# Optimization experiments

Measured on AMD Instinct MI355X. Metric: run time of the kernel, lower is better.

Reference implementation:

```python
import jax, jax.numpy as jnp
import numpy as np

B, S, D, H = 4, 2048, 1024, 16
DK = D // H
THETA = 10000.0


def _rope(x, pos):
    # x: [..., S, DK]; interleaved-pair rotation as in the torch module
    dk = x.shape[-1]
    inv_freq = 1.0 / (THETA ** (jnp.arange(0, dk, 2, dtype=jnp.float32) / dk))  # [dk/2]
    freqs = pos.astype(jnp.float32)[:, None] * inv_freq  # [S, dk/2]
    cos, sin = jnp.cos(freqs), jnp.sin(freqs)
    xr = x.reshape(*x.shape[:-1], dk // 2, 2)
    x0, x1 = xr[..., 0], xr[..., 1]
    rot = jnp.stack([x0 * cos - x1 * sin, x0 * sin + x1 * cos], axis=-1)
    return rot.reshape(x.shape)


def setup_inputs() -> dict:
    key = jax.random.key(0)
    ks = jax.random.split(key, 5)
    scale = 0.02
    return {
        "x": jax.random.normal(ks[0], (B, S, D), dtype=jnp.float32),
        "Wq": jax.random.normal(ks[1], (D, D), dtype=jnp.float32) * scale,
        "Wk": jax.random.normal(ks[2], (D, D), dtype=jnp.float32) * scale,
        "Wv": jax.random.normal(ks[3], (D, D), dtype=jnp.float32) * scale,
        "Wo": jax.random.normal(ks[4], (D, D), dtype=jnp.float32) * scale,
    }


def reference(x, Wq, Wk, Wv, Wo):
    b, s, d = x.shape
    pos = jnp.arange(s)
    # projections (Linear with no bias, y = x @ W^T)
    q = jnp.einsum('bsd,ed->bse', x, Wq).reshape(b, s, H, DK).transpose(0, 2, 1, 3)
    k = jnp.einsum('bsd,ed->bse', x, Wk).reshape(b, s, H, DK).transpose(0, 2, 1, 3)
    v = jnp.einsum('bsd,ed->bse', x, Wv).reshape(b, s, H, DK).transpose(0, 2, 1, 3)
    q = _rope(q, pos)
    k = _rope(k, pos)
    scores = jnp.einsum('bhqd,bhkd->bhqk', q, k) / jnp.sqrt(jnp.float32(DK))
    causal = jnp.tril(jnp.ones((s, s), dtype=bool))
    scores = jnp.where(causal, scores, -jnp.inf)
    attn = jax.nn.softmax(scores, axis=-1)
    out = jnp.einsum('bhqk,bhkd->bhqd', attn, v)
    out = out.transpose(0, 2, 1, 3).reshape(b, s, d)
    return jnp.einsum('bsd,ed->bse', out, Wo)
```

## Files before the change

### kernel.cpp

```cpp
#include <hip/hip_runtime.h>

#define B_  4
#define S_  2048
#define D_  1024
#define H_  16
#define DK_ 64
#define BH_ (B_*H_)
#define L2E 1.44269504088896f

typedef __attribute__((ext_vector_type(8))) short bf16x8;
typedef __attribute__((ext_vector_type(4))) float f32x4;
typedef __attribute__((ext_vector_type(16))) float f32x16;
typedef __attribute__((ext_vector_type(4))) unsigned u32x4;
typedef unsigned short u16;

__device__ __forceinline__ u16 f2bf(float f){
  unsigned u = __builtin_bit_cast(unsigned, f);
  u += 0x7fffu + ((u >> 16) & 1u);
  return (u16)(u >> 16);
}
__device__ __forceinline__ float bf2f(u16 h){
  unsigned u = ((unsigned)h) << 16;
  return __builtin_bit_cast(float, u);
}

#define GLD16(g,l) __builtin_amdgcn_global_load_lds( \
    (const __attribute__((address_space(1))) void*)(g), \
    (__attribute__((address_space(3))) void*)(l), 16, 0, 0)

#define MFMA16(a,b,c) __builtin_amdgcn_mfma_f32_16x16x32_bf16((a),(b),(c),0,0,0)
#define MFMA32(a,b,c) __builtin_amdgcn_mfma_f32_32x32x16_bf16((a),(b),(c),0,0,0)

__global__ void cast_kernel(const float4* __restrict__ in, ushort4* __restrict__ out, int n4){
  int i = blockIdx.x*blockDim.x + threadIdx.x;
  int stride = gridDim.x*blockDim.x;
  for (; i < n4; i += stride){
    float4 v = in[i];
    ushort4 o;
    o.x = f2bf(v.x); o.y = f2bf(v.y); o.z = f2bf(v.z); o.w = f2bf(v.w);
    out[i] = o;
  }
}

__global__ void trig_kernel(float* __restrict__ ct, float* __restrict__ st){
  int t = blockIdx.x*blockDim.x + threadIdx.x;
  int i = t & 31, s = t >> 5;
  float expo = -(float)(2*i) * (1.0f/(float)DK_);
  float inv = powf(10000.0f, expo);
  float ang = (float)s * inv;
  ct[t] = cosf(ang);
  st[t] = sinf(ang);
}

__global__ void rope_kernel(u16* __restrict__ X, const float* __restrict__ ct,
                            const float* __restrict__ st, float scale){
  int t = blockIdx.x*blockDim.x + threadIdx.x;
  int c8 = t & 7;
  int s  = (t >> 3) & (S_-1);
  bf16x8 v = *(bf16x8*)(X + (size_t)t*8);
  float4 c4 = *(const float4*)(ct + s*32 + c8*4);
  float4 s4 = *(const float4*)(st + s*32 + c8*4);
  float cc[4] = {c4.x, c4.y, c4.z, c4.w};
  float ss[4] = {s4.x, s4.y, s4.z, s4.w};
  #pragma unroll
  for (int j=0;j<4;++j){
    float x0 = bf2f((u16)v[2*j]);
    float x1 = bf2f((u16)v[2*j+1]);
    float r0 = x0*cc[j] - x1*ss[j];
    float r1 = x0*ss[j] + x1*cc[j];
    v[2*j]   = (short)f2bf(r0*scale);
    v[2*j+1] = (short)f2bf(r1*scale);
  }
  *(bf16x8*)(X + (size_t)t*8) = v;
}

template<int MODE>
__global__ __launch_bounds__(256, 2)
void gemm_bt(const u16* __restrict__ A,
             const u16* __restrict__ B0, const u16* __restrict__ B1, const u16* __restrict__ B2,
             u16* __restrict__ O0, u16* __restrict__ O1, u16* __restrict__ O2,
             float* __restrict__ Cf, int K){
  __shared__ __align__(16) u16 lA[128*64];
  __shared__ __align__(16) u16 lB[128*64];
  const u16* Bm = B0;
  u16* Om = O0;
  if (MODE == 0){
    if (blockIdx.z == 1){ Bm = B1; Om = O1; }
    else if (blockIdx.z == 2){ Bm = B2; Om = O2; }
  }
  const int m0 = blockIdx.y*128, n0 = blockIdx.x*128;
  const int tid = threadIdx.x, wave = tid>>6, lane = tid&63;
  const int wm = wave>>1, wn = wave&1;
  const int srow = lane>>3, scol = (lane&7)*8;

  f32x4 acc[4][4];
  #pragma unroll
  for (int m=0;m<4;++m)
    #pragma unroll
    for (int n=0;n<4;++n) acc[m][n] = (f32x4){0.f,0.f,0.f,0.f};

  #pragma unroll 1
  for (int k0 = 0; k0 < K; k0 += 64){
    #pragma unroll
    for (int j=0;j<4;++j){
      int rb = (wave*4 + j)*8;
      GLD16(A  + (size_t)(m0 + rb + srow)*K + k0 + scol, lA + rb*64);
      GLD16(Bm + (size_t)(n0 + rb + srow)*K + k0 + scol, lB + rb*64);
    }
    __syncthreads();
    #pragma unroll
    for (int kk=0;kk<2;++kk){
      bf16x8 af[4], bfr[4];
      #pragma unroll
      for (int m=0;m<4;++m) af[m]  = *(const bf16x8*)&lA[(wm*64 + m*16 + (lane&15))*64 + kk*32 + (lane>>4)*8];
      #pragma unroll
      for (int n=0;n<4;++n) bfr[n] = *(const bf16x8*)&lB[(wn*64 + n*16 + (lane&15))*64 + kk*32 + (lane>>4)*8];
      #pragma unroll
      for (int m=0;m<4;++m)
        #pragma unroll
        for (int n=0;n<4;++n)
          acc[m][n] = MFMA16(af[m], bfr[n], acc[m][n]);
    }
    __syncthreads();
  }

  #pragma unroll
  for (int m=0;m<4;++m){
    const int rb = m0 + wm*64 + m*16 + ((lane>>4)<<2);
    #pragma unroll
    for (int n=0;n<4;++n){
      const int e = n0 + wn*64 + n*16 + (lane&15);
      if (MODE == 0){
        const int h = e>>6, dk = e&63;
        if (blockIdx.z == 2){
          const int b = rb >> 11, s0 = rb & (S_-1);
          ushort4 w4;
          w4.x = f2bf(acc[m][n][0]); w4.y = f2bf(acc[m][n][1]);
          w4.z = f2bf(acc[m][n][2]); w4.w = f2bf(acc[m][n][3]);
          *(ushort4*)(Om + ((size_t)((b*H_ + h)*DK_ + dk))*S_ + s0) = w4;
        } else {
          #pragma unroll
          for (int r=0;r<4;++r){
            const int i = rb + r;
            const int b = i >> 11, s = i & (S_-1);
            Om[(size_t)((b*H_ + h)*S_ + s)*DK_ + dk] = f2bf(acc[m][n][r]);
          }
        }
      } else {
        #pragma unroll
        for (int r=0;r<4;++r)
          Cf[(size_t)(rb + r)*D_ + e] = acc[m][n][r];
      }
    }
  }
}

__global__ __launch_bounds__(256, 3)
void attn_kernel(const u16* __restrict__ Q, const u16* __restrict__ K,
                 const u16* __restrict__ Vt, u16* __restrict__ O){
  __shared__ __align__(16) u16 lK[64*64];
  __shared__ __align__(16) u16 lV[64*64];

  const int bh = blockIdx.x;
  const int qt = (int)(gridDim.y - 1 - blockIdx.y);
  const int b = bh >> 4, h = bh & 15;
  const int tid = threadIdx.x, wave = tid>>6, lane = tid&63;
  const int hi = lane >> 5, l31 = lane & 31;
  const int q0 = qt*128, qw = q0 + wave*32;
  const int qg = qw + l31;
  const u16* Qb = Q  + (size_t)bh*S_*DK_;
  const u16* Kb = K  + (size_t)bh*S_*DK_;
  const u16* Vb = Vt + (size_t)bh*DK_*S_;

  bf16x8 qf[4];
  #pragma unroll
  for (int ds=0; ds<4; ++ds)
    qf[ds] = *(const bf16x8*)(Qb + (size_t)qg*DK_ + ds*16 + hi*8);

  f32x16 oacc[2];
  oacc[0] = (f32x16)0.f; oacc[1] = (f32x16)0.f;
  float m_run = -1e30f, l_run = 0.f;

  const int srow8 = lane >> 3;
  const int csw = ((lane&7) ^ srow8) << 3;

  const int kv_end = (qt+1)*128;
  for (int kv0 = 0; kv0 < kv_end; kv0 += 64){
    #pragma unroll
    for (int it=0; it<2; ++it){
      const int rb = (it*4 + wave)*8;
      const int row = rb + srow8;
      GLD16(Kb + (size_t)(kv0+row)*DK_ + csw, lK + rb*64);
      GLD16(Vb + (size_t)row*S_ + kv0 + csw, lV + rb*64);
    }
    __syncthreads();

    if (kv0 < qw + 32){
      f32x16 sacc[2];
      sacc[0] = (f32x16)0.f; sacc[1] = (f32x16)0.f;
      __builtin_amdgcn_s_setprio(1);
      #pragma unroll
      for (int kb=0; kb<2; ++kb){
        const int krow = kb*32 + l31;
        #pragma unroll
        for (int ds=0; ds<4; ++ds){
          bf16x8 kf = *(const bf16x8*)&lK[krow*64 + (((ds*2+hi) ^ (krow&7))<<3)];
          sacc[kb] = MFMA32(kf, qf[ds], sacc[kb]);
        }
      }
      __builtin_amdgcn_s_setprio(0);

      if (kv0 + 63 > qw){
        #pragma unroll
        for (int kb=0; kb<2; ++kb)
          #pragma unroll
          for (int r=0; r<16; ++r){
            const int kvg = kv0 + kb*32 + 4*hi + (r&3) + 8*(r>>2);
            if (kvg > qg) sacc[kb][r] = -1e30f;
          }
      }

      float mx = sacc[0][0];
      #pragma unroll
      for (int r=1; r<16; ++r) mx = fmaxf(mx, sacc[0][r]);
      #pragma unroll
      for (int r=0; r<16; ++r) mx = fmaxf(mx, sacc[1][r]);
      mx = fmaxf(mx, __shfl_xor(mx, 32));
      const float mn = fmaxf(m_run, mx);
      const float alpha = exp2f((m_run - mn)*L2E);
      m_run = mn;
      const float nc = mn * L2E;
      float ps = 0.f;
      #pragma unroll
      for (int kb=0; kb<2; ++kb)
        #pragma unroll
        for (int r=0; r<16; ++r){
          float v = exp2f(__builtin_fmaf(sacc[kb][r], L2E, -nc));
          sacc[kb][r] = v;
          ps += v;
        }
      ps += __shfl_xor(ps, 32);
      l_run = l_run*alpha + ps;
      oacc[0] *= alpha;
      oacc[1] *= alpha;

      bf16x8 pa[4];
      #pragma unroll
      for (int kb=0; kb<2; ++kb){
        unsigned w[8];
        #pragma unroll
        for (int i=0; i<8; ++i){
          float a = sacc[kb][2*i], b2 = sacc[kb][2*i+1];
          asm("v_cvt_pk_bf16_f32 %0, %1, %2" : "=v"(w[i]) : "v"(a), "v"(b2));
        }
        auto s02 = __builtin_amdgcn_permlane32_swap(w[0], w[2], false, false);
        auto s13 = __builtin_amdgcn_permlane32_swap(w[1], w[3], false, false);
        auto s46 = __builtin_amdgcn_permlane32_swap(w[4], w[6], false, false);
        auto s57 = __builtin_amdgcn_permlane32_swap(w[5], w[7], false, false);
        u32x4 ua = {s02[0], s13[0], s02[1], s13[1]};
        u32x4 ub = {s46[0], s57[0], s46[1], s57[1]};
        pa[kb*2+0] = __builtin_bit_cast(bf16x8, ua);
        pa[kb*2+1] = __builtin_bit_cast(bf16x8, ub);
      }

      __builtin_amdgcn_s_setprio(1);
      #pragma unroll
      for (int dkb=0; dkb<2; ++dkb){
        const int vrow = dkb*32 + l31;
        #pragma unroll
        for (int ks=0; ks<4; ++ks){
          bf16x8 vf = *(const bf16x8*)&lV[vrow*64 + (((ks*2+hi) ^ (vrow&7))<<3)];
          oacc[dkb] = MFMA32(vf, pa[ks], oacc[dkb]);
        }
      }
      __builtin_amdgcn_s_setprio(0);
    }
    __syncthreads();
  }

  const float inv = 1.0f / l_run;
  #pragma unroll
  for (int dkb=0; dkb<2; ++dkb)
    #pragma unroll
    for (int rq=0; rq<4; ++rq){
      ushort4 w4;
      w4.x = f2bf(oacc[dkb][rq*4+0]*inv);
      w4.y = f2bf(oacc[dkb][rq*4+1]*inv);
      w4.z = f2bf(oacc[dkb][rq*4+2]*inv);
      w4.w = f2bf(oacc[dkb][rq*4+3]*inv);
      const int dk0 = dkb*32 + 8*rq + 4*hi;
      *(ushort4*)(O + (size_t)(b*S_+qg)*D_ + h*DK_ + dk0) = w4;
    }
}

extern "C" void kernel_launch(void* const* d_in, const int* in_sizes, int n_in,
                              void* d_out, int out_size, void* d_ws, size_t ws_size,
                              hipStream_t stream){
  const float* x  = (const float*)d_in[0];
  const float* Wq = (const float*)d_in[1];
  const float* Wk = (const float*)d_in[2];
  const float* Wv = (const float*)d_in[3];
  const float* Wo = (const float*)d_in[4];
  float* out = (float*)d_out;
  char* ws = (char*)d_ws;

  size_t off = 0;
  u16* xb  = (u16*)(ws + off); off += (size_t)B_*S_*D_*2;
  u16* wqb = (u16*)(ws + off); off += (size_t)D_*D_*2;
  u16* wkb = (u16*)(ws + off); off += (size_t)D_*D_*2;
  u16* wvb = (u16*)(ws + off); off += (size_t)D_*D_*2;
  u16* wob = (u16*)(ws + off); off += (size_t)D_*D_*2;
  u16* Qb  = (u16*)(ws + off); off += (size_t)BH_*S_*DK_*2;
  u16* Kb  = (u16*)(ws + off); off += (size_t)BH_*S_*DK_*2;
  u16* Vtb = (u16*)(ws + off); off += (size_t)BH_*S_*DK_*2;
  u16* Ob  = (u16*)(ws + off); off += (size_t)B_*S_*D_*2;
  float* ct = (float*)(ws + off); off += (size_t)S_*32*4;
  float* st = (float*)(ws + off); off += (size_t)S_*32*4;

  cast_kernel<<<2048,256,0,stream>>>((const float4*)x,  (ushort4*)xb,  B_*S_*D_/4);
  cast_kernel<<<512, 256,0,stream>>>((const float4*)Wq, (ushort4*)wqb, D_*D_/4);
  cast_kernel<<<512, 256,0,stream>>>((const float4*)Wk, (ushort4*)wkb, D_*D_/4);
  cast_kernel<<<512, 256,0,stream>>>((const float4*)Wv, (ushort4*)wvb, D_*D_/4);
  cast_kernel<<<512, 256,0,stream>>>((const float4*)Wo, (ushort4*)wob, D_*D_/4);
  trig_kernel<<<(S_*32)/256,256,0,stream>>>(ct, st);

  gemm_bt<0><<<dim3(8,64,3),256,0,stream>>>(xb, wqb,wkb,wvb, Qb,Kb,Vtb, nullptr, D_);

  rope_kernel<<<(BH_*S_*8)/256,256,0,stream>>>(Qb, ct, st, 0.125f);
  rope_kernel<<<(BH_*S_*8)/256,256,0,stream>>>(Kb, ct, st, 1.0f);

  attn_kernel<<<dim3(BH_, S_/128),256,0,stream>>>(Qb, Kb, Vtb, Ob);

  gemm_bt<1><<<dim3(8,64,1),256,0,stream>>>(Ob, wob,wob,wob, nullptr,nullptr,nullptr, out, D_);
}
```

Measured before the change: 210.0 us.

## Fuse RoPE into QKV GEMM epilogue, double-buffer attention KV, lazy rescale

Moves the RoPE rotation and Q scaling into the QKV projection epilogue. The accumulator tile is staged through shared memory so each thread can apply the rotation to 8 contiguous elements and write them with vectorized stores. This removes two rope kernel launches and their extra read/write of Q and K. The attention kernel now double-buffers K/V tiles in shared memory, prefetching the next tile while computing the current one, and raises its occupancy hint from 3 to 4. It also skips the online-softmax rescale unless the running max grows by more than a threshold, which trades exactness of the max subtraction for less work and risks overflow only in extreme cases.

```diff
diff --git a/kernel.cpp b/kernel.cpp
--- a/kernel.cpp
+++ b/kernel.cpp
@@ -52,36 +52,16 @@
   st[t] = sinf(ang);
 }
 
-__global__ void rope_kernel(u16* __restrict__ X, const float* __restrict__ ct,
-                            const float* __restrict__ st, float scale){
-  int t = blockIdx.x*blockDim.x + threadIdx.x;
-  int c8 = t & 7;
-  int s  = (t >> 3) & (S_-1);
-  bf16x8 v = *(bf16x8*)(X + (size_t)t*8);
-  float4 c4 = *(const float4*)(ct + s*32 + c8*4);
-  float4 s4 = *(const float4*)(st + s*32 + c8*4);
-  float cc[4] = {c4.x, c4.y, c4.z, c4.w};
-  float ss[4] = {s4.x, s4.y, s4.z, s4.w};
-  #pragma unroll
-  for (int j=0;j<4;++j){
-    float x0 = bf2f((u16)v[2*j]);
-    float x1 = bf2f((u16)v[2*j+1]);
-    float r0 = x0*cc[j] - x1*ss[j];
-    float r1 = x0*ss[j] + x1*cc[j];
-    v[2*j]   = (short)f2bf(r0*scale);
-    v[2*j+1] = (short)f2bf(r1*scale);
-  }
-  *(bf16x8*)(X + (size_t)t*8) = v;
-}
-
 template<int MODE>
 __global__ __launch_bounds__(256, 2)
 void gemm_bt(const u16* __restrict__ A,
              const u16* __restrict__ B0, const u16* __restrict__ B1, const u16* __restrict__ B2,
              u16* __restrict__ O0, u16* __restrict__ O1, u16* __restrict__ O2,
-             float* __restrict__ Cf, int K){
-  __shared__ __align__(16) u16 lA[128*64];
-  __shared__ __align__(16) u16 lB[128*64];
+             float* __restrict__ Cf,
+             const float* __restrict__ ct, const float* __restrict__ st, int K){
+  __shared__ __align__(16) u16 lAB[2*128*64];
+  u16* const lA = lAB;
+  u16* const lB = lAB + 128*64;
   const u16* Bm = B0;
   u16* Om = O0;
   if (MODE == 0){
@@ -124,15 +104,52 @@
     __syncthreads();
   }
 
-  #pragma unroll
-  for (int m=0;m<4;++m){
-    const int rb = m0 + wm*64 + m*16 + ((lane>>4)<<2);
-    #pragma unroll
-    for (int n=0;n<4;++n){
-      const int e = n0 + wn*64 + n*16 + (lane&15);
-      if (MODE == 0){
-        const int h = e>>6, dk = e&63;
-        if (blockIdx.z == 2){
+  if (MODE == 0 && blockIdx.z != 2){
+    const float scale = (blockIdx.z == 0) ? 0.125f : 1.0f;
+    #pragma unroll
+    for (int m=0;m<4;++m){
+      const int lr0 = wm*64 + m*16 + ((lane>>4)<<2);
+      #pragma unroll
+      for (int n=0;n<4;++n){
+        const int lc = wn*64 + n*16 + (lane&15);
+        #pragma unroll
+        for (int r=0;r<4;++r){
+          const int lr = lr0 + r;
+          lAB[lr*128 + (lc ^ (((lr>>2)&7)<<4))] = f2bf(acc[m][n][r]);
+        }
+      }
+    }
+    __syncthreads();
+    #pragma unroll
+    for (int k=0;k<8;++k){
+      const int cid = k*256 + tid;
+      const int rr = cid >> 4, cc = cid & 15;
+      bf16x8 v = *(const bf16x8*)&lAB[rr*128 + ((cc*8) ^ (((rr>>2)&7)<<4))];
+      const int i = m0 + rr, bb = i >> 11, s = i & (S_-1);
+      const int e0 = n0 + cc*8, h = e0 >> 6, dk0 = e0 & 63;
+      const float4 c4 = *(const float4*)(ct + s*32 + (dk0>>1));
+      const float4 s4 = *(const float4*)(st + s*32 + (dk0>>1));
+      const float cc4[4] = {c4.x,c4.y,c4.z,c4.w};
+      const float ss4[4] = {s4.x,s4.y,s4.z,s4.w};
+      bf16x8 o;
+      #pragma unroll
+      for (int j=0;j<4;++j){
+        const float x0 = bf2f((u16)v[2*j]);
+        const float x1 = bf2f((u16)v[2*j+1]);
+        o[2*j]   = (short)f2bf((x0*cc4[j] - x1*ss4[j])*scale);
+        o[2*j+1] = (short)f2bf((x0*ss4[j] + x1*cc4[j])*scale);
+      }
+      *(bf16x8*)(Om + ((size_t)((bb*H_ + h)*S_ + s))*DK_ + dk0) = o;
+    }
+  } else {
+    #pragma unroll
+    for (int m=0;m<4;++m){
+      const int rb = m0 + wm*64 + m*16 + ((lane>>4)<<2);
+      #pragma unroll
+      for (int n=0;n<4;++n){
+        const int e = n0 + wn*64 + n*16 + (lane&15);
+        if (MODE == 0){
+          const int h = e>>6, dk = e&63;
           const int b = rb >> 11, s0 = rb & (S_-1);
           ushort4 w4;
           w4.x = f2bf(acc[m][n][0]); w4.y = f2bf(acc[m][n][1]);
@@ -140,26 +157,19 @@
           *(ushort4*)(Om + ((size_t)((b*H_ + h)*DK_ + dk))*S_ + s0) = w4;
         } else {
           #pragma unroll
-          for (int r=0;r<4;++r){
-            const int i = rb + r;
-            const int b = i >> 11, s = i & (S_-1);
-            Om[(size_t)((b*H_ + h)*S_ + s)*DK_ + dk] = f2bf(acc[m][n][r]);
-          }
-        }
-      } else {
-        #pragma unroll
-        for (int r=0;r<4;++r)
-          Cf[(size_t)(rb + r)*D_ + e] = acc[m][n][r];
-      }
-    }
-  }
-}
-
-__global__ __launch_bounds__(256, 3)
+          for (int r=0;r<4;++r)
+            Cf[(size_t)(rb + r)*D_ + e] = acc[m][n][r];
+        }
+      }
+    }
+  }
+}
+
+__global__ __launch_bounds__(256, 4)
 void attn_kernel(const u16* __restrict__ Q, const u16* __restrict__ K,
                  const u16* __restrict__ Vt, u16* __restrict__ O){
-  __shared__ __align__(16) u16 lK[64*64];
-  __shared__ __align__(16) u16 lV[64*64];
+  __shared__ __align__(16) u16 lK[2][64*64];
+  __shared__ __align__(16) u16 lV[2][64*64];
 
   const int bh = blockIdx.x;
   const int qt = (int)(gridDim.y - 1 - blockIdx.y);
@@ -185,15 +195,28 @@
   const int csw = ((lane&7) ^ srow8) << 3;
 
   const int kv_end = (qt+1)*128;
+
+  #pragma unroll
+  for (int it=0; it<2; ++it){
+    const int rb = (it*4 + wave)*8;
+    const int row = rb + srow8;
+    GLD16(Kb + (size_t)row*DK_ + csw, lK[0] + rb*64);
+    GLD16(Vb + (size_t)row*S_ + csw,  lV[0] + rb*64);
+  }
+  __syncthreads();
+
+  int cur = 0;
   for (int kv0 = 0; kv0 < kv_end; kv0 += 64){
-    #pragma unroll
-    for (int it=0; it<2; ++it){
-      const int rb = (it*4 + wave)*8;
-      const int row = rb + srow8;
-      GLD16(Kb + (size_t)(kv0+row)*DK_ + csw, lK + rb*64);
-      GLD16(Vb + (size_t)row*S_ + kv0 + csw, lV + rb*64);
-    }
-    __syncthreads();
+    const int nxt = kv0 + 64;
+    if (nxt < kv_end){
+      #pragma unroll
+      for (int it=0; it<2; ++it){
+        const int rb = (it*4 + wave)*8;
+        const int row = rb + srow8;
+        GLD16(Kb + (size_t)(nxt+row)*DK_ + csw, lK[cur^1] + rb*64);
+        GLD16(Vb + (size_t)row*S_ + nxt + csw,  lV[cur^1] + rb*64);
+      }
+    }
 
     if (kv0 < qw + 32){
       f32x16 sacc[2];
@@ -204,7 +227,7 @@
         const int krow = kb*32 + l31;
         #pragma unroll
         for (int ds=0; ds<4; ++ds){
-          bf16x8 kf = *(const bf16x8*)&lK[krow*64 + (((ds*2+hi) ^ (krow&7))<<3)];
+          bf16x8 kf = *(const bf16x8*)&lK[cur][krow*64 + (((ds*2+hi) ^ (krow&7))<<3)];
           sacc[kb] = MFMA32(kf, qf[ds], sacc[kb]);
         }
       }
@@ -226,10 +249,15 @@
       #pragma unroll
       for (int r=0; r<16; ++r) mx = fmaxf(mx, sacc[1][r]);
       mx = fmaxf(mx, __shfl_xor(mx, 32));
-      const float mn = fmaxf(m_run, mx);
-      const float alpha = exp2f((m_run - mn)*L2E);
-      m_run = mn;
-      const float nc = mn * L2E;
+      if (!__all((mx - m_run)*L2E <= 8.0f)){
+        const float mn = fmaxf(m_run, mx);
+        const float alpha = exp2f((m_run - mn)*L2E);
+        m_run = mn;
+        l_run *= alpha;
+        oacc[0] *= alpha;
+        oacc[1] *= alpha;
+      }
+      const float nc = m_run * L2E;
       float ps = 0.f;
       #pragma unroll
       for (int kb=0; kb<2; ++kb)
@@ -240,9 +268,7 @@
           ps += v;
         }
       ps += __shfl_xor(ps, 32);
-      l_run = l_run*alpha + ps;
-      oacc[0] *= alpha;
-      oacc[1] *= alpha;
+      l_run += ps;
 
       bf16x8 pa[4];
       #pragma unroll
@@ -269,13 +295,14 @@
         const int vrow = dkb*32 + l31;
         #pragma unroll
         for (int ks=0; ks<4; ++ks){
-          bf16x8 vf = *(const bf16x8*)&lV[vrow*64 + (((ks*2+hi) ^ (vrow&7))<<3)];
+          bf16x8 vf = *(const bf16x8*)&lV[cur][vrow*64 + (((ks*2+hi) ^ (vrow&7))<<3)];
           oacc[dkb] = MFMA32(vf, pa[ks], oacc[dkb]);
         }
       }
       __builtin_amdgcn_s_setprio(0);
     }
     __syncthreads();
+    cur ^= 1;
   }
 
   const float inv = 1.0f / l_run;
@@ -324,12 +351,9 @@
   cast_kernel<<<512, 256,0,stream>>>((const float4*)Wo, (ushort4*)wob, D_*D_/4);
   trig_kernel<<<(S_*32)/256,256,0,stream>>>(ct, st);
 
-  gemm_bt<0><<<dim3(8,64,3),256,0,stream>>>(xb, wqb,wkb,wvb, Qb,Kb,Vtb, nullptr, D_);
-
-  rope_kernel<<<(BH_*S_*8)/256,256,0,stream>>>(Qb, ct, st, 0.125f);
-  rope_kernel<<<(BH_*S_*8)/256,256,0,stream>>>(Kb, ct, st, 1.0f);
+  gemm_bt<0><<<dim3(8,64,3),256,0,stream>>>(xb, wqb,wkb,wvb, Qb,Kb,Vtb, nullptr, ct, st, D_);
 
   attn_kernel<<<dim3(BH_, S_/128),256,0,stream>>>(Qb, Kb, Vtb, Ob);
 
-  gemm_bt<1><<<dim3(8,64,1),256,0,stream>>>(Ob, wob,wob,wob, nullptr,nullptr,nullptr, out, D_);
-}
+  gemm_bt<1><<<dim3(8,64,1),256,0,stream>>>(Ob, wob,wob,wob, nullptr,nullptr,nullptr, out, nullptr, nullptr, D_);
+}
```

Result: faster. 198.6 us (-5.4%).
